# Optimization experiments

Measured on AMD Instinct MI355X. Metric: run time of the kernel, lower is better.

Reference implementation:

```python
import jax, jax.numpy as jnp
import numpy as np

N_SPECIES = 4; N_BASIS = 128; N_GRAPH = 16; R_MAX = 6.0
NS_NODE, NV_NODE = 32, 16          # node irreps 32x0e + 16x1o
NS_EDGE = 16                       # initial edge irreps 16x0e
NS_OUT, NV_OUT = 16, 8             # output irreps 16x0e + 8x1o
NS_IN = 2 * NS_NODE + NS_EDGE      # 80 concatenated scalars
NV_IN = 2 * NV_NODE                # 32 concatenated vectors
NS_CONV = NS_OUT + NV_OUT          # 24 scalars (16 features + 8 gates)
W_SIZES = [NS_IN * NS_CONV, NS_IN * NV_OUT, NV_IN * NV_OUT, NV_IN * NS_CONV, NV_IN * NV_OUT]
N_NODES, N_EDGES = 8192, 65536
EPS = 1e-5


def gaussian_basis(d, stop, n):
    offsets = jnp.linspace(0.0, stop, n)
    coeff = -0.5 / (offsets[1] - offsets[0]) ** 2
    return jnp.exp(coeff * (d[:, None] - offsets[None, :]) ** 2)


def seg_mean(vals, seg, cnt):
    return jax.ops.segment_sum(vals, seg, num_segments=N_GRAPH) / cnt[:, None]


def setup_inputs():
    key = jax.random.key(0)
    ks = jax.random.split(key, 20)
    rn = lambda k, shape, scale: jax.random.normal(k, shape, jnp.float32) * scale
    inp = {}
    inp["node_fea"] = rn(ks[0], (N_NODES, NS_NODE + 3 * NV_NODE), 1.0)
    d = 0.5 + 5.0 * jax.random.uniform(ks[1], (N_EDGES,), jnp.float32)
    vec = jax.random.normal(ks[2], (N_EDGES, 3), jnp.float32)
    inp["edge_attr"] = jnp.concatenate([d[:, None], vec], axis=1)
    inp["edge_index"] = jax.random.randint(ks[3], (2, N_EDGES), 0, N_NODES)
    inp["x"] = jax.random.randint(ks[4], (N_NODES,), 0, N_SPECIES)
    inp["batch"] = jnp.sort(jax.random.randint(ks[5], (N_NODES,), 0, N_GRAPH))
    inp["w_rh"] = rn(ks[6], (N_BASIS, 64), N_BASIS ** -0.5); inp["b_rh"] = jnp.zeros((64,), jnp.float32)
    inp["w_ro"] = rn(ks[7], (64, sum(W_SIZES)), 64 ** -0.5); inp["b_ro"] = jnp.zeros((sum(W_SIZES),), jnp.float32)
    inp["w_pre"] = rn(ks[8], (NS_EDGE, NS_EDGE), NS_EDGE ** -0.5); inp["b_pre"] = jnp.zeros((NS_EDGE,), jnp.float32)
    inp["w_sc"] = rn(ks[9], (NS_EDGE, N_SPECIES ** 2, NS_OUT), 1.0)
    inp["w_post_s"] = rn(ks[10], (NS_OUT, NS_OUT), NS_OUT ** -0.5); inp["b_post_s"] = jnp.zeros((NS_OUT,), jnp.float32)
    inp["w_post_v"] = rn(ks[11], (NV_OUT, NV_OUT), NV_OUT ** -0.5)
    inp["ln_w_s"] = jnp.ones((NS_OUT,), jnp.float32); inp["ln_b_s"] = jnp.zeros((NS_OUT,), jnp.float32)
    inp["ln_w_v"] = jnp.ones((NV_OUT,), jnp.float32)
    inp["w_skip"] = rn(ks[12], (NS_EDGE, NS_OUT), NS_EDGE ** -0.5)
    inp["w_edge_s"] = rn(ks[13], (NS_OUT, NS_OUT), NS_OUT ** -0.5); inp["b_edge_s"] = jnp.zeros((NS_OUT,), jnp.float32)
    inp["w_edge_v"] = rn(ks[14], (NV_OUT, NV_OUT), NV_OUT ** -0.5)
    return inp


def _forward(node_fea, edge_attr, w_rh, b_rh, w_ro, b_ro, w_pre, b_pre, w_sc,
             w_post_s, b_post_s, w_post_v, ln_w_s, ln_b_s, ln_w_v,
             w_skip, w_edge_s, b_edge_s, w_edge_v, edge_index, x, batch):
    E = edge_index.shape[1]
    idx_i, idx_j = edge_index[0], edge_index[1]
    one_hot = jax.nn.one_hot(N_SPECIES * x[idx_i] + x[idx_j], N_SPECIES ** 2, dtype=node_fea.dtype)
    d, vec = edge_attr[:, 0], edge_attr[:, 1:4]
    u = vec / (jnp.linalg.norm(vec, axis=1, keepdims=True) + 1e-12)
    Y1 = np.sqrt(3.0) * u                                   # l=1 sph harm, component norm; Y0 == 1
    rbf = gaussian_basis(d, R_MAX, N_BASIS)                 # edge_length_embedded
    edge_s0 = gaussian_basis(d, 6.0, NS_EDGE)               # distance_expansion -> initial edge scalars
    # self connection: edge scalars x species-pair one-hot -> output scalars
    sc = jnp.einsum('ei,ej,ijo->eo', edge_s0, one_hot, w_sc) / np.sqrt(NS_EDGE * N_SPECIES ** 2)
    edge_s = edge_s0 @ w_pre + b_pre                        # lin_pre
    # gather node features by edge indices and concat
    nf_i, nf_j = node_fea[idx_i], node_fea[idx_j]
    s_in = jnp.concatenate([nf_i[:, :NS_NODE], nf_j[:, :NS_NODE], edge_s], axis=1)  # [E,80]
    v_in = jnp.concatenate([nf_i[:, NS_NODE:].reshape(E, NV_NODE, 3),
                            nf_j[:, NS_NODE:].reshape(E, NV_NODE, 3)], axis=1)      # [E,32,3]
    # radial MLP -> per-edge tensor-product path weights
    h = jax.nn.silu(rbf @ w_rh + b_rh)
    w_all = h @ w_ro + b_ro                                 # [E, 3840]
    w1, w2, w3, w4, w5 = jnp.split(w_all, np.cumsum(W_SIZES)[:-1].tolist(), axis=1)
    # equivariant tensor-product paths (explicit l<=1 Clebsch-Gordan structure)
    s0 = jnp.einsum('ei,eio->eo', s_in, w1.reshape(E, NS_IN, NS_CONV)) / np.sqrt(NS_IN)            # 0e x 0e -> 0e
    vA = jnp.einsum('ei,eio,ec->eoc', s_in, w2.reshape(E, NS_IN, NV_OUT), Y1) / np.sqrt(NS_IN)     # 0e x 1o -> 1o
    vB = jnp.einsum('eic,eio->eoc', v_in, w3.reshape(E, NV_IN, NV_OUT)) / np.sqrt(NV_IN)           # 1o x 0e -> 1o
    s1 = jnp.einsum('eic,eio,ec->eo', v_in, w4.reshape(E, NV_IN, NS_CONV), Y1) / np.sqrt(3.0 * NV_IN)  # 1o.1o -> 0e
    vC = jnp.einsum('eic,eio->eoc', jnp.cross(v_in, Y1[:, None, :]), w5.reshape(E, NV_IN, NV_OUT)) / np.sqrt(2.0 * NV_IN)  # 1o x 1o -> 1o
    s_conv = s0 + s1                                        # [E,24]
    v_conv = vA + vB + vC                                   # [E,8,3]
    # gate nonlinearity inside conv
    s_out = jax.nn.silu(s_conv[:, :NS_OUT])
    v_out = v_conv * jax.nn.sigmoid(s_conv[:, NS_OUT:])[:, :, None]
    # lin_post then self connection
    s_out = s_out @ w_post_s + b_post_s + sc
    v_out = jnp.einsum('eic,io->eoc', v_out, w_post_v)
    # e3LayerNorm keyed by graph id of source node
    eb = batch[idx_i]
    cnt = jnp.maximum(jax.ops.segment_sum(jnp.ones((E,), s_out.dtype), eb, num_segments=N_GRAPH), 1.0)
    mu = seg_mean(s_out, eb, cnt)
    s_c = s_out - mu[eb]
    rms_s = jnp.sqrt(seg_mean(s_c ** 2, eb, cnt).mean(axis=1, keepdims=True) + EPS)
    s_n = s_c / rms_s[eb] * ln_w_s + ln_b_s
    rms_v = jnp.sqrt((seg_mean((v_out ** 2).sum(-1), eb, cnt) / 3.0).mean(axis=1, keepdims=True) + EPS)
    v_n = v_out / rms_v[eb][:, :, None] * ln_w_v[None, :, None]
    # skip connection from old edge features (scalars only)
    s_n = s_n + edge_s0 @ w_skip
    # final lin_edge
    s_fin = s_n @ w_edge_s + b_edge_s
    v_fin = jnp.einsum('eic,io->eoc', v_n, w_edge_v)
    return jnp.concatenate([s_fin, v_fin.reshape(E, NV_OUT * 3)], axis=1)  # [E,40]


def reference(node_fea, edge_attr, edge_index, x, batch, w_rh, b_rh, w_ro, b_ro,
              w_pre, b_pre, w_sc, w_post_s, b_post_s, w_post_v, ln_w_s, ln_b_s, ln_w_v,
              w_skip, w_edge_s, b_edge_s, w_edge_v):
    return _forward(node_fea, edge_attr, w_rh, b_rh, w_ro, b_ro, w_pre, b_pre, w_sc,
                    w_post_s, b_post_s, w_post_v, ln_w_s, ln_b_s, ln_w_v,
                    w_skip, w_edge_s, b_edge_s, w_edge_v, edge_index, x, batch)
```

## Files before the change

kernel.cpp:

```cpp
#include <hip/hip_runtime.h>

typedef unsigned short u16;
typedef unsigned int u32;
typedef __attribute__((ext_vector_type(8))) _Float16 half8;
typedef __attribute__((ext_vector_type(2))) __fp16 fp16x2;
typedef __attribute__((ext_vector_type(4))) float floatx4;

#define E_TOTAL 65536

__device__ __forceinline__ u32 pk16(float x0, float x1) {
    union { fp16x2 h; u32 u; } c;
    c.h = __builtin_amdgcn_cvt_pkrtz(x0, x1);
    return c.u;
}
union Frag8h { u32 u[4]; half8 v; };


__global__ __launch_bounds__(1024) void k_init(float* __restrict__ ws, int* __restrict__ binv) {
    const int tid = threadIdx.x;
    for (int i = tid; i < 6144; i += 1024) ws[i] = 0.0f;
    if (tid < 64) {
        const int lane = tid;
        const int q = lane >> 4;
        if (lane < 32) binv[lane] = lane;
        half8 bfr;
        #pragma unroll
        for (int j = 0; j < 8; ++j) bfr[j] = (_Float16)(float)(q*8 + j + 1);
        #pragma unroll
        for (int s = 0; s < 32; ++s) {
            const int qa = s >> 3, ja = s & 7;
            half8 afr;
            #pragma unroll
            for (int j = 0; j < 8; ++j) afr[j] = (_Float16)0.0f;
            if (q == qa) afr[ja] = (_Float16)1.0f;
            floatx4 dc = {0.0f, 0.0f, 0.0f, 0.0f};
            dc = __builtin_amdgcn_mfma_f32_16x16x32_f16(afr, bfr, dc, 0, 0, 0);
            if (lane == 0) {
                const int sB = (int)(dc[0] + 0.5f) - 1;
                if (sB >= 0 && sB < 32) binv[sB] = s;
            }
        }
    }
}

__global__ __launch_bounds__(256) void k_edge_heavy(
    const float* __restrict__ node_fea, const float* __restrict__ edge_attr,
    const int* __restrict__ edge_index, const int* __restrict__ xsp,
    const float* __restrict__ w_rh, const float* __restrict__ b_rh,
    const float* __restrict__ w_ro, const float* __restrict__ b_ro,
    const float* __restrict__ w_pre, const float* __restrict__ b_pre,
    const float* __restrict__ w_sc, const float* __restrict__ w_post_s,
    const float* __restrict__ b_post_s, const float* __restrict__ w_post_v,
    const int* __restrict__ binv, const int* __restrict__ batch,
    float* __restrict__ ws_stats,
    float* __restrict__ out)
{
    __shared__ __align__(16) float sh_wt[32][130];
    __shared__ float sh_sin[32][80];
    __shared__ float sh_vl[32][3][32];
    __shared__ float sh_acc[32][56];
    __shared__ float sh_y1[32][4];
    __shared__ int   sh_kmap[32];

    u16*   a_rbf = (u16*)&sh_wt[0][0];
    u16*   a_h   = (u16*)((char*)&sh_wt[0][0] + 8192);
    float* es0f  = (float*)((char*)&sh_wt[0][0] + 12288);

    const int tid = threadIdx.x;
    const int ed = tid >> 4, l16 = tid & 15;
    const int lane = tid & 63, w = tid >> 6;
    const int quad = lane >> 4, l15 = lane & 15;
    const int e0 = blockIdx.x * 32 + ed;
    const int e1 = e0 + 16;

    if (tid < 32) sh_kmap[tid] = binv[tid];

    const int ni0 = edge_index[e0], nj0 = edge_index[E_TOTAL + e0];
    const int ni1 = edge_index[e1], nj1 = edge_index[E_TOTAL + e1];
    const float4 ea0 = *(const float4*)(edge_attr + 4*e0);
    const float4 ea1 = *(const float4*)(edge_attr + 4*e1);
    const float d0 = ea0.x, d1 = ea1.x;
    {
        const float invn0 = 1.0f / (sqrtf(ea0.y*ea0.y + ea0.z*ea0.z + ea0.w*ea0.w) + 1e-12f);
        const float invn1 = 1.0f / (sqrtf(ea1.y*ea1.y + ea1.z*ea1.z + ea1.w*ea1.w) + 1e-12f);
        if (l16 == 0) {
            sh_y1[ed][0]    = 1.7320508075688772f * ea0.y * invn0;
            sh_y1[ed][1]    = 1.7320508075688772f * ea0.z * invn0;
            sh_y1[ed][2]    = 1.7320508075688772f * ea0.w * invn0;
            sh_y1[16+ed][0] = 1.7320508075688772f * ea1.y * invn1;
            sh_y1[16+ed][1] = 1.7320508075688772f * ea1.z * invn1;
            sh_y1[16+ed][2] = 1.7320508075688772f * ea1.w * invn1;
        }
    }

    const float C128 = -0.5f * (127.0f/6.0f) * (127.0f/6.0f);
    const float S128 = 6.0f/127.0f;
    {
        Frag8h t0, t1;
        #pragma unroll
        for (int r2 = 0; r2 < 4; ++r2) {
            const int b0i = l16*8 + 2*r2;
            const float u0 = d0 - S128 * (float)b0i;
            const float u1 = d0 - S128 * (float)(b0i + 1);
            const float v0 = d1 - S128 * (float)b0i;
            const float v1 = d1 - S128 * (float)(b0i + 1);
            t0.u[r2] = pk16(expf(C128*u0*u0), expf(C128*u1*u1));
            t1.u[r2] = pk16(expf(C128*v0*v0), expf(C128*v1*v1));
        }
        *(half8*)&a_rbf[(l16*16 + ed)*8]        = t0.v;
        *(half8*)&a_rbf[2048 + (l16*16 + ed)*8] = t1.v;
    }
    {
        const float t0 = d0 - 0.4f * (float)l16;
        const float t1 = d1 - 0.4f * (float)l16;
        es0f[ed*16 + l16]      = expf(-3.125f * t0 * t0);
        es0f[(16+ed)*16 + l16] = expf(-3.125f * t1 * t1);
    }

    const float rs80 = 0.11180339887498949f;
    const float rs32 = 0.17677669529663689f;
    {
        const float* fi = node_fea + (size_t)ni0 * 80;
        const float* fj = node_fea + (size_t)nj0 * 80;
        sh_sin[ed][2*l16+0]    = fi[2*l16+0] * rs80;
        sh_sin[ed][2*l16+1]    = fi[2*l16+1] * rs80;
        sh_sin[ed][32+2*l16+0] = fj[2*l16+0] * rs80;
        sh_sin[ed][32+2*l16+1] = fj[2*l16+1] * rs80;
        #pragma unroll
        for (int c = 0; c < 3; ++c) {
            sh_vl[ed][c][l16]      = fi[32 + 3*l16 + c] * rs32;
            sh_vl[ed][c][16 + l16] = fj[32 + 3*l16 + c] * rs32;
        }
    }
    {
        const float* fi = node_fea + (size_t)ni1 * 80;
        const float* fj = node_fea + (size_t)nj1 * 80;
        sh_sin[16+ed][2*l16+0]    = fi[2*l16+0] * rs80;
        sh_sin[16+ed][2*l16+1]    = fi[2*l16+1] * rs80;
        sh_sin[16+ed][32+2*l16+0] = fj[2*l16+0] * rs80;
        sh_sin[16+ed][32+2*l16+1] = fj[2*l16+1] * rs80;
        #pragma unroll
        for (int c = 0; c < 3; ++c) {
            sh_vl[16+ed][c][l16]      = fi[32 + 3*l16 + c] * rs32;
            sh_vl[16+ed][c][16 + l16] = fj[32 + 3*l16 + c] * rs32;
        }
    }
    for (int s = tid; s < 32*56; s += 256) (&sh_acc[0][0])[s] = 0.0f;
    __syncthreads();

    int km[8];
    u32 voff0[8], voff1[8];
    #pragma unroll
    for (int j = 0; j < 8; ++j) {
        km[j] = sh_kmap[quad*8 + j];
        voff0[j] = (u32)(km[j] * 3840 + l15);
        voff1[j] = voff0[j] + 32u * 3840u;
    }

    float my_sc0, my_sc1;
    {
        const int o = l16;
        float es0v = b_pre[o], sc0 = 0.0f;
        float es1v = b_pre[o], sc1 = 0.0f;
        const int p0 = 4*xsp[ni0] + xsp[nj0];
        const int p1 = 4*xsp[ni1] + xsp[nj1];
        #pragma unroll
        for (int i = 0; i < 16; ++i) {
            const float g0 = es0f[ed*16 + i];
            const float g1 = es0f[(16+ed)*16 + i];
            es0v += g0 * w_pre[i*16 + o];
            es1v += g1 * w_pre[i*16 + o];
            sc0  += g0 * w_sc[(i*16 + p0)*16 + o];
            sc1  += g1 * w_sc[(i*16 + p1)*16 + o];
        }
        sh_sin[ed][64 + o]    = es0v * rs80;
        sh_sin[16+ed][64 + o] = es1v * rs80;
        my_sc0 = sc0 * 0.0625f;
        my_sc1 = sc1 * 0.0625f;
    }

    {
        floatx4 h0 = {0.0f, 0.0f, 0.0f, 0.0f};
        floatx4 h1 = {0.0f, 0.0f, 0.0f, 0.0f};
        #pragma unroll
        for (int kk = 0; kk < 4; ++kk) {
            const half8 ag0 = *(const half8*)&a_rbf[((kk*4 + quad)*16 + l15)*8];
            const half8 ag1 = *(const half8*)&a_rbf[2048 + ((kk*4 + quad)*16 + l15)*8];
            Frag8h bh;
            #pragma unroll
            for (int jj = 0; jj < 4; ++jj) {
                const float x0 = w_rh[(size_t)(kk*32 + km[2*jj+0])*64 + w*16 + l15];
                const float x1 = w_rh[(size_t)(kk*32 + km[2*jj+1])*64 + w*16 + l15];
                bh.u[jj] = pk16(x0, x1);
            }
            h0 = __builtin_amdgcn_mfma_f32_16x16x32_f16(ag0, bh.v, h0, 0, 0, 0);
            h1 = __builtin_amdgcn_mfma_f32_16x16x32_f16(ag1, bh.v, h1, 0, 0, 0);
        }
        const int hn = w*16 + l15;
        const float bb = b_rh[hn];
        const int k8 = hn >> 3, j2 = hn & 7;
        #pragma unroll
        for (int r = 0; r < 4; ++r) {
            const int m = quad*4 + r;
            {
                const float x = h0[r] + bb;
                const float s = x / (1.0f + expf(-x));
                union { _Float16 h; u16 u; } cv; cv.h = (_Float16)s;
                a_h[(k8*16 + m)*8 + j2] = cv.u;
            }
            {
                const float x = h1[r] + bb;
                const float s = x / (1.0f + expf(-x));
                union { _Float16 h; u16 u; } cv; cv.h = (_Float16)s;
                a_h[1024 + (k8*16 + m)*8 + j2] = cv.u;
            }
        }
    }
    __syncthreads();

    const half8 a0g0 = *(const half8*)&a_h[((0*4 + quad)*16 + l15)*8];
    const half8 a1g0 = *(const half8*)&a_h[((1*4 + quad)*16 + l15)*8];
    const half8 a0g1 = *(const half8*)&a_h[1024 + ((0*4 + quad)*16 + l15)*8];
    const half8 a1g1 = *(const half8*)&a_h[1024 + ((1*4 + quad)*16 + l15)*8];

    float pf[32];
    float pbias[2];
    #pragma unroll
    for (int ct = 0; ct < 2; ++ct) {
        const int sgct = __builtin_amdgcn_readfirstlane(w*2 + ct);
        const float* bp = w_ro + sgct*16;
        #pragma unroll
        for (int j = 0; j < 8; ++j) {
            pf[ct*16 + j]     = bp[voff0[j]];
            pf[ct*16 + 8 + j] = bp[voff1[j]];
        }
        pbias[ct] = b_ro[sgct*16 + l15];
    }

    for (int ch = 0; ch < 30; ++ch) {
        const int coff = ch * 128;
        floatx4 acc0[2], acc1[2];
        float bias[2];
        #pragma unroll
        for (int ct = 0; ct < 2; ++ct) {
            Frag8h b0, b1;
            #pragma unroll
            for (int jj = 0; jj < 4; ++jj) {
                b0.u[jj] = pk16(pf[ct*16 + 2*jj],     pf[ct*16 + 2*jj+1]);
                b1.u[jj] = pk16(pf[ct*16 + 8 + 2*jj], pf[ct*16 + 8 + 2*jj+1]);
            }
            floatx4 a = {0.0f, 0.0f, 0.0f, 0.0f};
            a = __builtin_amdgcn_mfma_f32_16x16x32_f16(a0g0, b0.v, a, 0, 0, 0);
            a = __builtin_amdgcn_mfma_f32_16x16x32_f16(a1g0, b1.v, a, 0, 0, 0);
            acc0[ct] = a;
            floatx4 c = {0.0f, 0.0f, 0.0f, 0.0f};
            c = __builtin_amdgcn_mfma_f32_16x16x32_f16(a0g1, b0.v, c, 0, 0, 0);
            c = __builtin_amdgcn_mfma_f32_16x16x32_f16(a1g1, b1.v, c, 0, 0, 0);
            acc1[ct] = c;
            bias[ct] = pbias[ct];
        }
        __syncthreads();
        #pragma unroll
        for (int ct = 0; ct < 2; ++ct) {
            const int col = w*32 + ct*16 + l15;
            #pragma unroll
            for (int r = 0; r < 4; ++r) {
                sh_wt[quad*4 + r][col]      = acc0[ct][r] + bias[ct];
                sh_wt[16 + quad*4 + r][col] = acc1[ct][r] + bias[ct];
            }
        }
        __syncthreads();

        if (ch < 29) {
            #pragma unroll
            for (int ct = 0; ct < 2; ++ct) {
                const int sgct = __builtin_amdgcn_readfirstlane((ch+1)*8 + w*2 + ct);
                const float* bp = w_ro + sgct*16;
                #pragma unroll
                for (int j = 0; j < 8; ++j) {
                    pf[ct*16 + j]     = bp[voff0[j]];
                    pf[ct*16 + 8 + j] = bp[voff1[j]];
                }
                pbias[ct] = b_ro[sgct*16 + l15];
            }
        }

        if (ch < 15) {
            for (int idx = tid; idx < 768; idx += 256) {
                const int eo = idx / 24, o = idx % 24;
                const int i0 = (coff > o) ? (coff - o + 23) / 24 : 0;
                int i1 = (coff + 128 - o + 23) / 24; if (i1 > 80) i1 = 80;
                float a = 0.0f;
                for (int i = i0; i < i1; ++i)
                    a += sh_sin[eo][i] * sh_wt[eo][i*24 + o - coff];
                sh_acc[eo][o] += a;
            }
        } else if (ch < 20) {
            const int ib = (ch - 15) * 16;
            for (int idx = tid; idx < 256; idx += 256) {
                const int eo = idx >> 3, o = idx & 7;
                float a = 0.0f;
                #pragma unroll
                for (int i = 0; i < 16; ++i)
                    a += sh_sin[eo][ib + i] * sh_wt[eo][i*8 + o];
                sh_acc[eo][24 + o] += a;
            }
        } else if (ch < 22) {
            const int ib = (ch - 20) * 16;
            for (int idx = tid; idx < 768; idx += 256) {
                const int eo = idx / 24, rem = idx % 24;
                const int o = rem / 3, cc = rem % 3;
                float a = 0.0f;
                #pragma unroll
                for (int i = 0; i < 16; ++i)
                    a += sh_vl[eo][cc][ib + i] * sh_wt[eo][i*8 + o];
                sh_acc[eo][32 + o*3 + cc] += a;
            }
        } else if (ch < 28) {
            const int rel = coff - 2816;
            for (int idx = tid; idx < 768; idx += 256) {
                const int eo = idx / 24, o = idx % 24;
                const int i0 = (rel > o) ? (rel - o + 23) / 24 : 0;
                int i1 = (rel + 128 - o + 23) / 24; if (i1 > 32) i1 = 32;
                const float Ya = sh_y1[eo][0], Yb = sh_y1[eo][1], Yc = sh_y1[eo][2];
                float a = 0.0f;
                for (int i = i0; i < i1; ++i) {
                    const float qv = sh_vl[eo][0][i]*Ya + sh_vl[eo][1][i]*Yb
                                   + sh_vl[eo][2][i]*Yc;
                    a += qv * sh_wt[eo][i*24 + o - rel];
                }
                sh_acc[eo][o] += a * 0.57735026918962573f;
            }
        } else {
            const int ib = (ch - 28) * 16;
            for (int idx = tid; idx < 768; idx += 256) {
                const int eo = idx / 24, rem = idx % 24;
                const int o = rem / 3, cc = rem % 3;
                const int c1 = (cc < 2) ? cc + 1 : 0;
                const int c2 = (c1 < 2) ? c1 + 1 : 0;
                const float Yp = sh_y1[eo][c2];
                const float Ym = sh_y1[eo][c1];
                float a = 0.0f;
                #pragma unroll
                for (int i = 0; i < 16; ++i)
                    a += (sh_vl[eo][c1][ib+i]*Yp - sh_vl[eo][c2][ib+i]*Ym) * sh_wt[eo][i*8 + o];
                sh_acc[eo][32 + o*3 + cc] += a * 0.70710678118654746f;
            }
        }
    }
    __syncthreads();

    float* bins = &sh_wt[0][0];
    for (int s = tid; s < 768; s += 256) bins[s] = 0.0f;
    __syncthreads();

    const int gi0 = batch[ni0];
    const int gi1 = batch[ni1];
    #pragma unroll
    for (int g = 0; g < 2; ++g) {
        const int er = g*16 + ed;
        const int e  = (g == 0) ? e0 : e1;
        const int gi = (g == 0) ? gi0 : gi1;
        const float msc = (g == 0) ? my_sc0 : my_sc1;
        {
            const int o = l16;
            float a = b_post_s[o] + msc;
            #pragma unroll
            for (int i = 0; i < 16; ++i) {
                const float sv = sh_acc[er][i];
                a += (sv / (1.0f + expf(-sv))) * w_post_s[i*16 + o];
            }
            out[(size_t)e*40 + o] = a;
            atomicAdd(&bins[gi*48 + o], a);
            atomicAdd(&bins[gi*48 + 16 + o], a*a);
            if (o == 0) atomicAdd(&bins[gi*48 + 40], 1.0f);
        }
        if (l16 < 8) {
            const int o = l16;
            const float Ya = sh_y1[er][0], Yb = sh_y1[er][1], Yc = sh_y1[er][2];
            float r0 = 0.0f, r1 = 0.0f, r2 = 0.0f;
            #pragma unroll
            for (int i = 0; i < 8; ++i) {
                const float gt = 1.0f / (1.0f + expf(-sh_acc[er][16 + i]));
                const float a2 = sh_acc[er][24 + i];
                const float ww = w_post_v[i*8 + o];
                r0 += (a2*Ya + sh_acc[er][32 + i*3 + 0]) * gt * ww;
                r1 += (a2*Yb + sh_acc[er][32 + i*3 + 1]) * gt * ww;
                r2 += (a2*Yc + sh_acc[er][32 + i*3 + 2]) * gt * ww;
            }
            out[(size_t)e*40 + 16 + o*3 + 0] = r0;
            out[(size_t)e*40 + 16 + o*3 + 1] = r1;
            out[(size_t)e*40 + 16 + o*3 + 2] = r2;
            atomicAdd(&bins[gi*48 + 32 + o], r0*r0 + r1*r1 + r2*r2);
        }
    }
    __syncthreads();
    {
        float* rep = ws_stats + (blockIdx.x & 7) * 768;
        for (int s = tid; s < 768; s += 256) {
            const float x = bins[s];
            if (x != 0.0f) atomicAdd(&rep[s], x);
        }
    }
}

__global__ __launch_bounds__(256) void k_edge_final(
    float* buf, const float* __restrict__ ws,
    const float* __restrict__ edge_attr, const int* __restrict__ edge_index,
    const int* __restrict__ batch,
    const float* __restrict__ ln_w_s, const float* __restrict__ ln_b_s,
    const float* __restrict__ ln_w_v, const float* __restrict__ w_skip,
    const float* __restrict__ w_edge_s, const float* __restrict__ b_edge_s,
    const float* __restrict__ w_edge_v)
{
    __shared__ float sh_mu[16][16];
    __shared__ float sh_is[16], sh_iv[16];
    __shared__ float sh_lws[16], sh_lbs[16], sh_lwv[8];
    __shared__ float sh_skip[16][16], sh_wes[16][16], sh_bes[16], sh_wev[8][8];
    const int tid = threadIdx.x;
    if (tid < 16) {
        const int g = tid;
        float sums[41];
        #pragma unroll
        for (int k = 0; k < 41; ++k) sums[k] = 0.0f;
        for (int r = 0; r < 8; ++r) {
            const float* rep = ws + r*768 + g*48;
            for (int chn = 0; chn < 16; ++chn) { sums[chn] += rep[chn]; sums[16+chn] += rep[16+chn]; }
            for (int o = 0; o < 8; ++o) sums[32+o] += rep[32+o];
            sums[40] += rep[40];
        }
        float cnt = sums[40]; if (cnt < 1.0f) cnt = 1.0f;
        const float ic = 1.0f / cnt;
        float vs = 0.0f;
        for (int chn = 0; chn < 16; ++chn) {
            const float mu = sums[chn] * ic;
            sh_mu[g][chn] = mu;
            vs += sums[16+chn] * ic - mu * mu;
        }
        if (vs < 0.0f) vs = 0.0f;
        sh_is[g] = 1.0f / sqrtf(vs * (1.0f/16.0f) + 1e-5f);
        float vv = 0.0f;
        for (int o = 0; o < 8; ++o) vv += sums[32+o];
        vv = vv * ic * (1.0f/3.0f) * (1.0f/8.0f);
        sh_iv[g] = 1.0f / sqrtf(vv + 1e-5f);
    }
    sh_skip[tid >> 4][tid & 15] = w_skip[tid];
    sh_wes[tid >> 4][tid & 15]  = w_edge_s[tid];
    if (tid < 16) {
        sh_lws[tid] = ln_w_s[tid];
        sh_lbs[tid] = ln_b_s[tid];
        sh_bes[tid] = b_edge_s[tid];
    }
    if (tid < 8)  sh_lwv[tid] = ln_w_v[tid];
    if (tid < 64) sh_wev[tid >> 3][tid & 7] = w_edge_v[tid];
    __syncthreads();

    const int e = blockIdx.x * 256 + tid;
    const int g = batch[edge_index[e]];
    const float d = edge_attr[4*e];
    float es0[16];
    #pragma unroll
    for (int b = 0; b < 16; ++b) {
        const float t = d - 0.4f * (float)b;
        es0[b] = expf(-3.125f * t * t);
    }
    float p[40];
    float* pb = buf + (size_t)e * 40;
    #pragma unroll
    for (int j = 0; j < 40; ++j) p[j] = pb[j];

    const float is = sh_is[g];
    float sn[16];
    #pragma unroll
    for (int chn = 0; chn < 16; ++chn)
        sn[chn] = (p[chn] - sh_mu[g][chn]) * is * sh_lws[chn] + sh_lbs[chn];
    #pragma unroll
    for (int b = 0; b < 16; ++b) {
        const float g0 = es0[b];
        #pragma unroll
        for (int chn = 0; chn < 16; ++chn) sn[chn] += g0 * sh_skip[b][chn];
    }
    #pragma unroll
    for (int o = 0; o < 16; ++o) {
        float a = sh_bes[o];
        #pragma unroll
        for (int chn = 0; chn < 16; ++chn) a += sn[chn] * sh_wes[chn][o];
        pb[o] = a;
    }
    const float iv = sh_iv[g];
    float vn[8][3];
    #pragma unroll
    for (int i = 0; i < 8; ++i) {
        const float f = iv * sh_lwv[i];
        vn[i][0] = p[16 + i*3 + 0] * f;
        vn[i][1] = p[16 + i*3 + 1] * f;
        vn[i][2] = p[16 + i*3 + 2] * f;
    }
    #pragma unroll
    for (int o = 0; o < 8; ++o) {
        float r0 = 0.0f, r1 = 0.0f, r2 = 0.0f;
        #pragma unroll
        for (int i = 0; i < 8; ++i) {
            const float w = sh_wev[i][o];
            r0 += vn[i][0] * w; r1 += vn[i][1] * w; r2 += vn[i][2] * w;
        }
        pb[16 + o*3 + 0] = r0;
        pb[16 + o*3 + 1] = r1;
        pb[16 + o*3 + 2] = r2;
    }
}

extern "C" void kernel_launch(void* const* d_in, const int* in_sizes, int n_in,
                              void* d_out, int out_size, void* d_ws, size_t ws_size,
                              hipStream_t stream)
{
    const float* node_fea  = (const float*)d_in[0];
    const float* edge_attr = (const float*)d_in[1];
    const int* edge_index  = (const int*)d_in[2];
    const int* xsp         = (const int*)d_in[3];
    const int* batch       = (const int*)d_in[4];
    const float* w_rh      = (const float*)d_in[5];
    const float* b_rh      = (const float*)d_in[6];
    const float* w_ro      = (const float*)d_in[7];
    const float* b_ro      = (const float*)d_in[8];
    const float* w_pre     = (const float*)d_in[9];
    const float* b_pre     = (const float*)d_in[10];
    const float* w_sc      = (const float*)d_in[11];
    const float* w_post_s  = (const float*)d_in[12];
    const float* b_post_s  = (const float*)d_in[13];
    const float* w_post_v  = (const float*)d_in[14];
    const float* ln_w_s    = (const float*)d_in[15];
    const float* ln_b_s    = (const float*)d_in[16];
    const float* ln_w_v    = (const float*)d_in[17];
    const float* w_skip    = (const float*)d_in[18];
    const float* w_edge_s  = (const float*)d_in[19];
    const float* b_edge_s  = (const float*)d_in[20];
    const float* w_edge_v  = (const float*)d_in[21];

    float* ws   = (float*)d_ws;
    int*   binv = (int*)(ws + 6144);
    float* out  = (float*)d_out;

    k_init<<<1, 1024, 0, stream>>>(ws, binv);
    k_edge_heavy<<<2048, 256, 0, stream>>>(node_fea, edge_attr, edge_index, xsp,
        w_rh, b_rh, w_ro, b_ro, w_pre, b_pre, w_sc, w_post_s, b_post_s, w_post_v,
        binv, batch, ws, out);
    k_edge_final<<<256, 256, 0, stream>>>(out, ws, edge_attr, edge_index,
        batch, ln_w_s, ln_b_s, ln_w_v, w_skip, w_edge_s, b_edge_s, w_edge_v);
}
```

Baseline: 408.8 us.

## Process 64 edges per 512-thread block to halve per-edge weight-generation loads

Each block now handles 64 edges with 512 threads instead of 32 edges with 256. Each wave produces one 16-column tile per chunk across four 16-edge groups, rather than two tiles across two groups. This halves how often each w_ro weight slice is loaded from global memory and packed to fp16 per edge, and spreads the per-chunk contraction over twice as many threads. In exchange, shared memory per block roughly doubles and the block launch size grows, which may lower occupancy and make the per-chunk barriers more expensive.

```diff
diff --git a/kernel.cpp b/kernel.cpp
--- a/kernel.cpp
+++ b/kernel.cpp
@@ -43,7 +43,7 @@
     }
 }
 
-__global__ __launch_bounds__(256) void k_edge_heavy(
+__global__ __launch_bounds__(512) void k_edge_heavy(
     const float* __restrict__ node_fea, const float* __restrict__ edge_attr,
     const int* __restrict__ edge_index, const int* __restrict__ xsp,
     const float* __restrict__ w_rh, const float* __restrict__ b_rh,
@@ -55,97 +55,92 @@
     float* __restrict__ ws_stats,
     float* __restrict__ out)
 {
-    __shared__ __align__(16) float sh_wt[32][130];
-    __shared__ float sh_sin[32][80];
-    __shared__ float sh_vl[32][3][32];
-    __shared__ float sh_acc[32][56];
-    __shared__ float sh_y1[32][4];
+    __shared__ __align__(16) float sh_wt[64][130];
+    __shared__ float sh_sin[64][80];
+    __shared__ float sh_vl[64][3][32];
+    __shared__ float sh_acc[64][56];
+    __shared__ float sh_y1[64][4];
     __shared__ int   sh_kmap[32];
 
     u16*   a_rbf = (u16*)&sh_wt[0][0];
-    u16*   a_h   = (u16*)((char*)&sh_wt[0][0] + 8192);
-    float* es0f  = (float*)((char*)&sh_wt[0][0] + 12288);
+    u16*   a_h   = (u16*)((char*)&sh_wt[0][0] + 16384);
+    float* es0f  = (float*)((char*)&sh_wt[0][0] + 24576);
 
     const int tid = threadIdx.x;
-    const int ed = tid >> 4, l16 = tid & 15;
+    const int ed2 = tid >> 4, l16 = tid & 15;
     const int lane = tid & 63, w = tid >> 6;
     const int quad = lane >> 4, l15 = lane & 15;
-    const int e0 = blockIdx.x * 32 + ed;
-    const int e1 = e0 + 16;
 
     if (tid < 32) sh_kmap[tid] = binv[tid];
-
-    const int ni0 = edge_index[e0], nj0 = edge_index[E_TOTAL + e0];
-    const int ni1 = edge_index[e1], nj1 = edge_index[E_TOTAL + e1];
-    const float4 ea0 = *(const float4*)(edge_attr + 4*e0);
-    const float4 ea1 = *(const float4*)(edge_attr + 4*e1);
-    const float d0 = ea0.x, d1 = ea1.x;
-    {
-        const float invn0 = 1.0f / (sqrtf(ea0.y*ea0.y + ea0.z*ea0.z + ea0.w*ea0.w) + 1e-12f);
-        const float invn1 = 1.0f / (sqrtf(ea1.y*ea1.y + ea1.z*ea1.z + ea1.w*ea1.w) + 1e-12f);
-        if (l16 == 0) {
-            sh_y1[ed][0]    = 1.7320508075688772f * ea0.y * invn0;
-            sh_y1[ed][1]    = 1.7320508075688772f * ea0.z * invn0;
-            sh_y1[ed][2]    = 1.7320508075688772f * ea0.w * invn0;
-            sh_y1[16+ed][0] = 1.7320508075688772f * ea1.y * invn1;
-            sh_y1[16+ed][1] = 1.7320508075688772f * ea1.z * invn1;
-            sh_y1[16+ed][2] = 1.7320508075688772f * ea1.w * invn1;
-        }
-    }
 
     const float C128 = -0.5f * (127.0f/6.0f) * (127.0f/6.0f);
     const float S128 = 6.0f/127.0f;
+    const float rs80 = 0.11180339887498949f;
+    const float rs32 = 0.17677669529663689f;
+
+    int niA, njA, niB, njB;
+    float dA, dB;
     {
-        Frag8h t0, t1;
+        const int eA = blockIdx.x * 64 + ed2;
+        const int eB = eA + 32;
+        niA = edge_index[eA]; njA = edge_index[E_TOTAL + eA];
+        niB = edge_index[eB]; njB = edge_index[E_TOTAL + eB];
+        const float4 eaA = *(const float4*)(edge_attr + 4*eA);
+        const float4 eaB = *(const float4*)(edge_attr + 4*eB);
+        dA = eaA.x; dB = eaB.x;
+        const float invnA = 1.0f / (sqrtf(eaA.y*eaA.y + eaA.z*eaA.z + eaA.w*eaA.w) + 1e-12f);
+        const float invnB = 1.0f / (sqrtf(eaB.y*eaB.y + eaB.z*eaB.z + eaB.w*eaB.w) + 1e-12f);
+        if (l16 == 0) {
+            sh_y1[ed2][0]    = 1.7320508075688772f * eaA.y * invnA;
+            sh_y1[ed2][1]    = 1.7320508075688772f * eaA.z * invnA;
+            sh_y1[ed2][2]    = 1.7320508075688772f * eaA.w * invnA;
+            sh_y1[32+ed2][0] = 1.7320508075688772f * eaB.y * invnB;
+            sh_y1[32+ed2][1] = 1.7320508075688772f * eaB.z * invnB;
+            sh_y1[32+ed2][2] = 1.7320508075688772f * eaB.w * invnB;
+        }
+        const int gA = ed2 >> 4, mA = ed2 & 15;
+        const int gB = 2 + gA,   mB = mA;
+        Frag8h tA, tB;
         #pragma unroll
         for (int r2 = 0; r2 < 4; ++r2) {
             const int b0i = l16*8 + 2*r2;
-            const float u0 = d0 - S128 * (float)b0i;
-            const float u1 = d0 - S128 * (float)(b0i + 1);
-            const float v0 = d1 - S128 * (float)b0i;
-            const float v1 = d1 - S128 * (float)(b0i + 1);
-            t0.u[r2] = pk16(expf(C128*u0*u0), expf(C128*u1*u1));
-            t1.u[r2] = pk16(expf(C128*v0*v0), expf(C128*v1*v1));
-        }
-        *(half8*)&a_rbf[(l16*16 + ed)*8]        = t0.v;
-        *(half8*)&a_rbf[2048 + (l16*16 + ed)*8] = t1.v;
-    }
-    {
-        const float t0 = d0 - 0.4f * (float)l16;
-        const float t1 = d1 - 0.4f * (float)l16;
-        es0f[ed*16 + l16]      = expf(-3.125f * t0 * t0);
-        es0f[(16+ed)*16 + l16] = expf(-3.125f * t1 * t1);
-    }
-
-    const float rs80 = 0.11180339887498949f;
-    const float rs32 = 0.17677669529663689f;
-    {
-        const float* fi = node_fea + (size_t)ni0 * 80;
-        const float* fj = node_fea + (size_t)nj0 * 80;
-        sh_sin[ed][2*l16+0]    = fi[2*l16+0] * rs80;
-        sh_sin[ed][2*l16+1]    = fi[2*l16+1] * rs80;
-        sh_sin[ed][32+2*l16+0] = fj[2*l16+0] * rs80;
-        sh_sin[ed][32+2*l16+1] = fj[2*l16+1] * rs80;
+            const float u0 = dA - S128 * (float)b0i;
+            const float u1 = dA - S128 * (float)(b0i + 1);
+            const float v0 = dB - S128 * (float)b0i;
+            const float v1 = dB - S128 * (float)(b0i + 1);
+            tA.u[r2] = pk16(expf(C128*u0*u0), expf(C128*u1*u1));
+            tB.u[r2] = pk16(expf(C128*v0*v0), expf(C128*v1*v1));
+        }
+        *(half8*)&a_rbf[gA*2048 + (l16*16 + mA)*8] = tA.v;
+        *(half8*)&a_rbf[gB*2048 + (l16*16 + mB)*8] = tB.v;
+        const float t0 = dA - 0.4f * (float)l16;
+        const float t1 = dB - 0.4f * (float)l16;
+        es0f[ed2*16 + l16]      = expf(-3.125f * t0 * t0);
+        es0f[(32+ed2)*16 + l16] = expf(-3.125f * t1 * t1);
+
+        const float* fiA = node_fea + (size_t)niA * 80;
+        const float* fjA = node_fea + (size_t)njA * 80;
+        sh_sin[ed2][2*l16+0]    = fiA[2*l16+0] * rs80;
+        sh_sin[ed2][2*l16+1]    = fiA[2*l16+1] * rs80;
+        sh_sin[ed2][32+2*l16+0] = fjA[2*l16+0] * rs80;
+        sh_sin[ed2][32+2*l16+1] = fjA[2*l16+1] * rs80;
+        const float* fiB = node_fea + (size_t)niB * 80;
+        const float* fjB = node_fea + (size_t)njB * 80;
+        sh_sin[32+ed2][2*l16+0]    = fiB[2*l16+0] * rs80;
+        sh_sin[32+ed2][2*l16+1]    = fiB[2*l16+1] * rs80;
+        sh_sin[32+ed2][32+2*l16+0] = fjB[2*l16+0] * rs80;
+        sh_sin[32+ed2][32+2*l16+1] = fjB[2*l16+1] * rs80;
         #pragma unroll
         for (int c = 0; c < 3; ++c) {
-            sh_vl[ed][c][l16]      = fi[32 + 3*l16 + c] * rs32;
-            sh_vl[ed][c][16 + l16] = fj[32 + 3*l16 + c] * rs32;
-        }
-    }
-    {
-        const float* fi = node_fea + (size_t)ni1 * 80;
-        const float* fj = node_fea + (size_t)nj1 * 80;
-        sh_sin[16+ed][2*l16+0]    = fi[2*l16+0] * rs80;
-        sh_sin[16+ed][2*l16+1]    = fi[2*l16+1] * rs80;
-        sh_sin[16+ed][32+2*l16+0] = fj[2*l16+0] * rs80;
-        sh_sin[16+ed][32+2*l16+1] = fj[2*l16+1] * rs80;
-        #pragma unroll
-        for (int c = 0; c < 3; ++c) {
-            sh_vl[16+ed][c][l16]      = fi[32 + 3*l16 + c] * rs32;
-            sh_vl[16+ed][c][16 + l16] = fj[32 + 3*l16 + c] * rs32;
-        }
-    }
-    for (int s = tid; s < 32*56; s += 256) (&sh_acc[0][0])[s] = 0.0f;
+            sh_vl[ed2][c][l16]         = fiA[32 + 3*l16 + c] * rs32;
+            sh_vl[ed2][c][16 + l16]    = fjA[32 + 3*l16 + c] * rs32;
+            sh_vl[32+ed2][c][l16]      = fiB[32 + 3*l16 + c] * rs32;
+            sh_vl[32+ed2][c][16 + l16] = fjB[32 + 3*l16 + c] * rs32;
+        }
+    }
+    const int giA = batch[niA];
+    const int giB = batch[niB];
+    for (int s = tid; s < 64*56; s += 512) (&sh_acc[0][0])[s] = 0.0f;
     __syncthreads();
 
     int km[8];
@@ -157,46 +152,48 @@
         voff1[j] = voff0[j] + 32u * 3840u;
     }
 
-    float my_sc0, my_sc1;
+    float my_scA, my_scB;
     {
         const int o = l16;
-        float es0v = b_pre[o], sc0 = 0.0f;
-        float es1v = b_pre[o], sc1 = 0.0f;
-        const int p0 = 4*xsp[ni0] + xsp[nj0];
-        const int p1 = 4*xsp[ni1] + xsp[nj1];
+        float esA = b_pre[o], scA = 0.0f;
+        float esB = b_pre[o], scB = 0.0f;
+        const int pA = 4*xsp[niA] + xsp[njA];
+        const int pB = 4*xsp[niB] + xsp[njB];
         #pragma unroll
         for (int i = 0; i < 16; ++i) {
-            const float g0 = es0f[ed*16 + i];
-            const float g1 = es0f[(16+ed)*16 + i];
-            es0v += g0 * w_pre[i*16 + o];
-            es1v += g1 * w_pre[i*16 + o];
-            sc0  += g0 * w_sc[(i*16 + p0)*16 + o];
-            sc1  += g1 * w_sc[(i*16 + p1)*16 + o];
-        }
-        sh_sin[ed][64 + o]    = es0v * rs80;
-        sh_sin[16+ed][64 + o] = es1v * rs80;
-        my_sc0 = sc0 * 0.0625f;
-        my_sc1 = sc1 * 0.0625f;
+            const float g0 = es0f[ed2*16 + i];
+            const float g1 = es0f[(32+ed2)*16 + i];
+            esA += g0 * w_pre[i*16 + o];
+            esB += g1 * w_pre[i*16 + o];
+            scA += g0 * w_sc[(i*16 + pA)*16 + o];
+            scB += g1 * w_sc[(i*16 + pB)*16 + o];
+        }
+        sh_sin[ed2][64 + o]    = esA * rs80;
+        sh_sin[32+ed2][64 + o] = esB * rs80;
+        my_scA = scA * 0.0625f;
+        my_scB = scB * 0.0625f;
     }
 
     {
+        const int wl = w & 3, gpair = w >> 2;
+        const int G0 = gpair*2, G1 = G0 + 1;
         floatx4 h0 = {0.0f, 0.0f, 0.0f, 0.0f};
         floatx4 h1 = {0.0f, 0.0f, 0.0f, 0.0f};
         #pragma unroll
         for (int kk = 0; kk < 4; ++kk) {
-            const half8 ag0 = *(const half8*)&a_rbf[((kk*4 + quad)*16 + l15)*8];
-            const half8 ag1 = *(const half8*)&a_rbf[2048 + ((kk*4 + quad)*16 + l15)*8];
+            const half8 ag0 = *(const half8*)&a_rbf[G0*2048 + ((kk*4 + quad)*16 + l15)*8];
+            const half8 ag1 = *(const half8*)&a_rbf[G1*2048 + ((kk*4 + quad)*16 + l15)*8];
             Frag8h bh;
             #pragma unroll
             for (int jj = 0; jj < 4; ++jj) {
-                const float x0 = w_rh[(size_t)(kk*32 + km[2*jj+0])*64 + w*16 + l15];
-                const float x1 = w_rh[(size_t)(kk*32 + km[2*jj+1])*64 + w*16 + l15];
+                const float x0 = w_rh[(size_t)(kk*32 + km[2*jj+0])*64 + wl*16 + l15];
+                const float x1 = w_rh[(size_t)(kk*32 + km[2*jj+1])*64 + wl*16 + l15];
                 bh.u[jj] = pk16(x0, x1);
             }
             h0 = __builtin_amdgcn_mfma_f32_16x16x32_f16(ag0, bh.v, h0, 0, 0, 0);
             h1 = __builtin_amdgcn_mfma_f32_16x16x32_f16(ag1, bh.v, h1, 0, 0, 0);
         }
-        const int hn = w*16 + l15;
+        const int hn = wl*16 + l15;
         const float bb = b_rh[hn];
         const int k8 = hn >> 3, j2 = hn & 7;
         #pragma unroll
@@ -206,87 +203,84 @@
                 const float x = h0[r] + bb;
                 const float s = x / (1.0f + expf(-x));
                 union { _Float16 h; u16 u; } cv; cv.h = (_Float16)s;
-                a_h[(k8*16 + m)*8 + j2] = cv.u;
+                a_h[G0*1024 + (k8*16 + m)*8 + j2] = cv.u;
             }
             {
                 const float x = h1[r] + bb;
                 const float s = x / (1.0f + expf(-x));
                 union { _Float16 h; u16 u; } cv; cv.h = (_Float16)s;
-                a_h[1024 + (k8*16 + m)*8 + j2] = cv.u;
+                a_h[G1*1024 + (k8*16 + m)*8 + j2] = cv.u;
             }
         }
     }
     __syncthreads();
 
-    const half8 a0g0 = *(const half8*)&a_h[((0*4 + quad)*16 + l15)*8];
-    const half8 a1g0 = *(const half8*)&a_h[((1*4 + quad)*16 + l15)*8];
-    const half8 a0g1 = *(const half8*)&a_h[1024 + ((0*4 + quad)*16 + l15)*8];
-    const half8 a1g1 = *(const half8*)&a_h[1024 + ((1*4 + quad)*16 + l15)*8];
-
-    float pf[32];
-    float pbias[2];
-    #pragma unroll
-    for (int ct = 0; ct < 2; ++ct) {
-        const int sgct = __builtin_amdgcn_readfirstlane(w*2 + ct);
+    const half8 aA0 = *(const half8*)&a_h[0*1024 + ((0*4 + quad)*16 + l15)*8];
+    const half8 aA1 = *(const half8*)&a_h[0*1024 + ((1*4 + quad)*16 + l15)*8];
+    const half8 aB0 = *(const half8*)&a_h[1*1024 + ((0*4 + quad)*16 + l15)*8];
+    const half8 aB1 = *(const half8*)&a_h[1*1024 + ((1*4 + quad)*16 + l15)*8];
+    const half8 aC0 = *(const half8*)&a_h[2*1024 + ((0*4 + quad)*16 + l15)*8];
+    const half8 aC1 = *(const half8*)&a_h[2*1024 + ((1*4 + quad)*16 + l15)*8];
+    const half8 aD0 = *(const half8*)&a_h[3*1024 + ((0*4 + quad)*16 + l15)*8];
+    const half8 aD1 = *(const half8*)&a_h[3*1024 + ((1*4 + quad)*16 + l15)*8];
+
+    float pf[16];
+    float pbias;
+    {
+        const int sgct = __builtin_amdgcn_readfirstlane(w);
         const float* bp = w_ro + sgct*16;
         #pragma unroll
         for (int j = 0; j < 8; ++j) {
-            pf[ct*16 + j]     = bp[voff0[j]];
-            pf[ct*16 + 8 + j] = bp[voff1[j]];
-        }
-        pbias[ct] = b_ro[sgct*16 + l15];
+            pf[j]     = bp[voff0[j]];
+            pf[8 + j] = bp[voff1[j]];
+        }
+        pbias = b_ro[sgct*16 + l15];
     }
 
     for (int ch = 0; ch < 30; ++ch) {
         const int coff = ch * 128;
-        floatx4 acc0[2], acc1[2];
-        float bias[2];
-        #pragma unroll
-        for (int ct = 0; ct < 2; ++ct) {
-            Frag8h b0, b1;
-            #pragma unroll
-            for (int jj = 0; jj < 4; ++jj) {
-                b0.u[jj] = pk16(pf[ct*16 + 2*jj],     pf[ct*16 + 2*jj+1]);
-                b1.u[jj] = pk16(pf[ct*16 + 8 + 2*jj], pf[ct*16 + 8 + 2*jj+1]);
-            }
-            floatx4 a = {0.0f, 0.0f, 0.0f, 0.0f};
-            a = __builtin_amdgcn_mfma_f32_16x16x32_f16(a0g0, b0.v, a, 0, 0, 0);
-            a = __builtin_amdgcn_mfma_f32_16x16x32_f16(a1g0, b1.v, a, 0, 0, 0);
-            acc0[ct] = a;
-            floatx4 c = {0.0f, 0.0f, 0.0f, 0.0f};
-            c = __builtin_amdgcn_mfma_f32_16x16x32_f16(a0g1, b0.v, c, 0, 0, 0);
-            c = __builtin_amdgcn_mfma_f32_16x16x32_f16(a1g1, b1.v, c, 0, 0, 0);
-            acc1[ct] = c;
-            bias[ct] = pbias[ct];
-        }
+        Frag8h b0, b1;
+        #pragma unroll
+        for (int jj = 0; jj < 4; ++jj) {
+            b0.u[jj] = pk16(pf[2*jj],     pf[2*jj+1]);
+            b1.u[jj] = pk16(pf[8 + 2*jj], pf[8 + 2*jj+1]);
+        }
+        floatx4 accA = {0,0,0,0}, accB = {0,0,0,0}, accC = {0,0,0,0}, accD = {0,0,0,0};
+        accA = __builtin_amdgcn_mfma_f32_16x16x32_f16(aA0, b0.v, accA, 0, 0, 0);
+        accA = __builtin_amdgcn_mfma_f32_16x16x32_f16(aA1, b1.v, accA, 0, 0, 0);
+        accB = __builtin_amdgcn_mfma_f32_16x16x32_f16(aB0, b0.v, accB, 0, 0, 0);
+        accB = __builtin_amdgcn_mfma_f32_16x16x32_f16(aB1, b1.v, accB, 0, 0, 0);
+        accC = __builtin_amdgcn_mfma_f32_16x16x32_f16(aC0, b0.v, accC, 0, 0, 0);
+        accC = __builtin_amdgcn_mfma_f32_16x16x32_f16(aC1, b1.v, accC, 0, 0, 0);
+        accD = __builtin_amdgcn_mfma_f32_16x16x32_f16(aD0, b0.v, accD, 0, 0, 0);
+        accD = __builtin_amdgcn_mfma_f32_16x16x32_f16(aD1, b1.v, accD, 0, 0, 0);
+        const float bsv = pbias;
         __syncthreads();
-        #pragma unroll
-        for (int ct = 0; ct < 2; ++ct) {
-            const int col = w*32 + ct*16 + l15;
+        {
+            const int col = w*16 + l15;
             #pragma unroll
             for (int r = 0; r < 4; ++r) {
-                sh_wt[quad*4 + r][col]      = acc0[ct][r] + bias[ct];
-                sh_wt[16 + quad*4 + r][col] = acc1[ct][r] + bias[ct];
+                sh_wt[ 0 + quad*4 + r][col] = accA[r] + bsv;
+                sh_wt[16 + quad*4 + r][col] = accB[r] + bsv;
+                sh_wt[32 + quad*4 + r][col] = accC[r] + bsv;
+                sh_wt[48 + quad*4 + r][col] = accD[r] + bsv;
             }
         }
         __syncthreads();
 
         if (ch < 29) {
+            const int sgct = __builtin_amdgcn_readfirstlane((ch+1)*8 + w);
+            const float* bp = w_ro + sgct*16;
             #pragma unroll
-            for (int ct = 0; ct < 2; ++ct) {
-                const int sgct = __builtin_amdgcn_readfirstlane((ch+1)*8 + w*2 + ct);
-                const float* bp = w_ro + sgct*16;
-                #pragma unroll
-                for (int j = 0; j < 8; ++j) {
-                    pf[ct*16 + j]     = bp[voff0[j]];
-                    pf[ct*16 + 8 + j] = bp[voff1[j]];
-                }
-                pbias[ct] = b_ro[sgct*16 + l15];
-            }
+            for (int j = 0; j < 8; ++j) {
+                pf[j]     = bp[voff0[j]];
+                pf[8 + j] = bp[voff1[j]];
+            }
+            pbias = b_ro[sgct*16 + l15];
         }
 
         if (ch < 15) {
-            for (int idx = tid; idx < 768; idx += 256) {
+            for (int idx = tid; idx < 1536; idx += 512) {
                 const int eo = idx / 24, o = idx % 24;
                 const int i0 = (coff > o) ? (coff - o + 23) / 24 : 0;
                 int i1 = (coff + 128 - o + 23) / 24; if (i1 > 80) i1 = 80;
@@ -297,7 +291,7 @@
             }
         } else if (ch < 20) {
             const int ib = (ch - 15) * 16;
-            for (int idx = tid; idx < 256; idx += 256) {
+            for (int idx = tid; idx < 512; idx += 512) {
                 const int eo = idx >> 3, o = idx & 7;
                 float a = 0.0f;
                 #pragma unroll
@@ -307,7 +301,7 @@
             }
         } else if (ch < 22) {
             const int ib = (ch - 20) * 16;
-            for (int idx = tid; idx < 768; idx += 256) {
+            for (int idx = tid; idx < 1536; idx += 512) {
                 const int eo = idx / 24, rem = idx % 24;
                 const int o = rem / 3, cc = rem % 3;
                 float a = 0.0f;
@@ -318,7 +312,7 @@
             }
         } else if (ch < 28) {
             const int rel = coff - 2816;
-            for (int idx = tid; idx < 768; idx += 256) {
+            for (int idx = tid; idx < 1536; idx += 512) {
                 const int eo = idx / 24, o = idx % 24;
                 const int i0 = (rel > o) ? (rel - o + 23) / 24 : 0;
                 int i1 = (rel + 128 - o + 23) / 24; if (i1 > 32) i1 = 32;
@@ -333,7 +327,7 @@
             }
         } else {
             const int ib = (ch - 28) * 16;
-            for (int idx = tid; idx < 768; idx += 256) {
+            for (int idx = tid; idx < 1536; idx += 512) {
                 const int eo = idx / 24, rem = idx % 24;
                 const int o = rem / 3, cc = rem % 3;
                 const int c1 = (cc < 2) ? cc + 1 : 0;
@@ -351,17 +345,15 @@
     __syncthreads();
 
     float* bins = &sh_wt[0][0];
-    for (int s = tid; s < 768; s += 256) bins[s] = 0.0f;
+    for (int s = tid; s < 768; s += 512) bins[s] = 0.0f;
     __syncthreads();
 
-    const int gi0 = batch[ni0];
-    const int gi1 = batch[ni1];
-    #pragma unroll
-    for (int g = 0; g < 2; ++g) {
-        const int er = g*16 + ed;
-        const int e  = (g == 0) ? e0 : e1;
-        const int gi = (g == 0) ? gi0 : gi1;
-        const float msc = (g == 0) ? my_sc0 : my_sc1;
+    #pragma unroll
+    for (int gg = 0; gg < 2; ++gg) {
+        const int er = gg*32 + ed2;
+        const int e  = blockIdx.x * 64 + er;
+        const int gi = (gg == 0) ? giA : giB;
+        const float msc = (gg == 0) ? my_scA : my_scB;
         {
             const int o = l16;
             float a = b_post_s[o] + msc;
@@ -397,7 +389,7 @@
     __syncthreads();
     {
         float* rep = ws_stats + (blockIdx.x & 7) * 768;
-        for (int s = tid; s < 768; s += 256) {
+        for (int s = tid; s < 768; s += 512) {
             const float x = bins[s];
             if (x != 0.0f) atomicAdd(&rep[s], x);
         }
@@ -542,7 +534,7 @@
     float* out  = (float*)d_out;
 
     k_init<<<1, 1024, 0, stream>>>(ws, binv);
-    k_edge_heavy<<<2048, 256, 0, stream>>>(node_fea, edge_attr, edge_index, xsp,
+    k_edge_heavy<<<1024, 512, 0, stream>>>(node_fea, edge_attr, edge_index, xsp,
         w_rh, b_rh, w_ro, b_ro, w_pre, b_pre, w_sc, w_post_s, b_post_s, w_post_v,
         binv, batch, ws, out);
     k_edge_final<<<256, 256, 0, stream>>>(out, ws, edge_attr, edge_index,
```

After: 402.8 us (median of 2 runs). About the same (-1.5%).
